# Performance work log

Measured on AMD Instinct MI355X. Metric: run time of the kernel, lower is better.

Reference implementation:

```python
import jax, jax.numpy as jnp
import numpy as np

VOCAB, EMB, HID, NCLS, B, T = 50000, 32, 64, 3, 512, 512

def setup_inputs() -> dict:
    key = jax.random.key(0)
    ks = jax.random.split(key, 7)
    tokens = jax.random.randint(ks[0], (B, T), 0, VOCAB, dtype=jnp.int32)
    emb = jax.random.normal(ks[1], (VOCAB, EMB), dtype=jnp.float32) * 0.05
    # Keras LSTM weights: kernel [EMB, 4*HID], recurrent_kernel [HID, 4*HID], bias [4*HID]; gate order i,f,c,o
    Wk = jax.random.normal(ks[2], (EMB, 4 * HID), dtype=jnp.float32) * (1.0 / np.sqrt(EMB))
    Wr = jax.random.normal(ks[3], (HID, 4 * HID), dtype=jnp.float32) * (1.0 / np.sqrt(HID))
    b = jnp.zeros((4 * HID,), dtype=jnp.float32)
    Wd = jax.random.normal(ks[4], (HID, NCLS), dtype=jnp.float32) * (1.0 / np.sqrt(HID))
    bd = jnp.zeros((NCLS,), dtype=jnp.float32)
    return {"tokens": tokens, "emb": emb, "Wk": Wk, "Wr": Wr, "b": b, "Wd": Wd, "bd": bd}

def _lstm_last_hidden(x, Wk, Wr, b):
    # x: [B, T, EMB] -> last hidden state [B, HID]. Keras gate order: i, f, c(g), o.
    Bsz = x.shape[0]
    # Precompute input projections for all timesteps (one big GEMM): [T, B, 4H]
    xz = jnp.einsum('bte,eh->tbh', x, Wk) + b

    def step(carry, xzt):
        h, c = carry
        z = xzt + h @ Wr  # [B, 4H]
        i, f, g, o = jnp.split(z, 4, axis=-1)
        i = jax.nn.sigmoid(i)
        f = jax.nn.sigmoid(f)
        o = jax.nn.sigmoid(o)
        c = f * c + i * jnp.tanh(g)
        h = o * jnp.tanh(c)
        return (h, c), None

    h0 = jnp.zeros((Bsz, HID), dtype=x.dtype)
    c0 = jnp.zeros((Bsz, HID), dtype=x.dtype)
    (hT, _), _ = jax.lax.scan(step, (h0, c0), xz)
    return hT

def reference(tokens, emb, Wk, Wr, b, Wd, bd):
    x = emb[tokens]                      # [B, T, EMB] embedding lookup
    h = _lstm_last_hidden(x, Wk, Wr, b)  # [B, HID]
    # Dropout layers are identity at inference; Dense + softmax
    logits = h @ Wd + bd                 # [B, NCLS]
    return jax.nn.softmax(logits, axis=-1)
```

## Files before the change

### kernel.cpp

```cpp
#include <hip/hip_runtime.h>


#define VOCAB 50000
#define EMB 32
#define HID 64
#define NCLS 3
#define BATCH 512
#define TSEQ 512
#define FOURH 256
#define LOG2E 1.4426950408889634f
#define GSEQ 4
#define NBLK (BATCH / GSEQ)

typedef _Float16 half8 __attribute__((ext_vector_type(8)));
typedef float f32x4 __attribute__((ext_vector_type(4)));

#define MFMA16 __builtin_amdgcn_mfma_f32_16x16x32_f16
#define PKRTZ(a, b) __builtin_bit_cast(int, __builtin_amdgcn_cvt_pkrtz((a), (b)))

#define LSTM_STEP(CUR, TT, XW, XL)                                            \
    {                                                                         \
        const half8* ap = (const half8*)(hxc + (CUR) * 768 + abase);          \
        const half8 a0 = ap[0];                                               \
        const half8 a1 = ap[4];                                               \
        const half8 a2 = ap[8];                                               \
        if (li8) {                                                            \
            int2 st;                                                          \
            st.x = PKRTZ(XW.x, XW.y);                                         \
            st.y = PKRTZ(XW.z, XW.w);                                         \
            *(int2*)(hxc + ((CUR) ^ 1) * 768 + xwoff) = st;                   \
            const int tn2 = ((TT) + 2 < TSEQ) ? (TT) + 2 : TSEQ - 1;          \
            const int tk = toks[(w << 9) + tn2];                              \
            XL = *(const float4*)(emb + tk * EMB + (l << 2));                 \
        }                                                                     \
        f32x4 ac0, ac1, ac2, ac3;                                             \
        ac0 = MFMA16(a0, bfr[0][0], zz, 0, 0, 0);                             \
        ac1 = MFMA16(a0, bfr[1][0], zz, 0, 0, 0);                             \
        ac2 = MFMA16(a0, bfr[2][0], zz, 0, 0, 0);                             \
        ac3 = MFMA16(a0, bfr[3][0], zz, 0, 0, 0);                             \
        ac0 = MFMA16(a1, bfr[0][1], ac0, 0, 0, 0);                            \
        ac1 = MFMA16(a1, bfr[1][1], ac1, 0, 0, 0);                            \
        ac2 = MFMA16(a1, bfr[2][1], ac2, 0, 0, 0);                            \
        ac3 = MFMA16(a1, bfr[3][1], ac3, 0, 0, 0);                            \
        ac0 = MFMA16(a2, bfr[0][2], ac0, 0, 0, 0);                            \
        ac1 = MFMA16(a2, bfr[1][2], ac1, 0, 0, 0);                            \
        ac2 = MFMA16(a2, bfr[2][2], ac2, 0, 0, 0);                            \
        ac3 = MFMA16(a2, bfr[3][2], ac3, 0, 0, 0);                            \
        const float zi = ac0[0], zf = ac1[0], zg = ac2[0], zo = ac3[0];       \
        const float si = __builtin_amdgcn_rcpf(                               \
            1.0f + __builtin_amdgcn_exp2f(fmaf(zi, -LOG2E, bci)));            \
        const float sf = __builtin_amdgcn_rcpf(                               \
            1.0f + __builtin_amdgcn_exp2f(fmaf(zf, -LOG2E, bcf)));            \
        const float sg = __builtin_amdgcn_rcpf(                               \
            1.0f + __builtin_amdgcn_exp2f(fmaf(zg, -2.0f * LOG2E, bcg)));     \
        const float so = __builtin_amdgcn_rcpf(                               \
            1.0f + __builtin_amdgcn_exp2f(fmaf(zo, -LOG2E, bco)));            \
        const float gt = fmaf(2.0f, sg, -1.0f);                               \
        cst = fmaf(sf, cst, si * gt);                                         \
        const float st2 = __builtin_amdgcn_rcpf(                              \
            1.0f + __builtin_amdgcn_exp2f(cst * (-2.0f * LOG2E)));            \
        const float th = fmaf(2.0f, st2, -1.0f);                              \
        const float hv = so * th;                                             \
        *(_Float16*)(hxc + ((CUR) ^ 1) * 768 + hwoff) = (_Float16)hv;         \
        __syncthreads();                                                      \
    }

__global__ __launch_bounds__(256)
void lstm_kernel(const int* __restrict__ tokens, const float* __restrict__ emb,
                 const float* __restrict__ Wk, const float* __restrict__ Wr,
                 const float* __restrict__ bias, const float* __restrict__ Wd,
                 const float* __restrict__ bd, float* __restrict__ out)
{
    __shared__ __align__(16) _Float16 hx[2][GSEQ][96];
    __shared__ int toks[GSEQ * TSEQ];

    const int tid = threadIdx.x;
    const int w   = tid >> 6;
    const int l   = tid & 63;
    const int li  = l & 15;
    const int q   = l >> 4;
    const bool li8 = (l < 8);
    const int s0  = blockIdx.x << 2;

    char* hxc = (char*)&hx[0][0][0];

    {
        const int4* src = (const int4*)(tokens + (s0 << 9));
        int4* dst = (int4*)toks;
        dst[tid] = src[tid];
        dst[tid + 256] = src[tid + 256];
    }

    if (tid < 64) {
        int2 z2; z2.x = 0; z2.y = 0;
        *(int2*)(hxc + (tid >> 4) * 192 + ((tid & 15) << 3)) = z2;
    }

    half8 bfr[4][3];
#pragma unroll
    for (int g = 0; g < 4; ++g) {
        const int col = (g << 6) + (w << 4) + li;
#pragma unroll
        for (int c2 = 0; c2 < 3; ++c2) {
#pragma unroll
            for (int i = 0; i < 8; ++i) {
                const int k = (c2 << 5) + (q << 3) + i;
                const float wv = (k < HID) ? Wr[k * FOURH + col]
                                           : Wk[(k - HID) * FOURH + col];
                bfr[g][c2][i] = (_Float16)wv;
            }
        }
    }

    const int u = (w << 4) + li;
    const float bci = -bias[u] * LOG2E;
    const float bcf = -bias[u + 64] * LOG2E;
    const float bcg = -bias[u + 128] * (2.0f * LOG2E);
    const float bco = -bias[u + 192] * LOG2E;

    const int abase = ((li >> 2) * 192) + (q << 4);
    const int hwoff = q * 192 + (u << 1);
    const int xwoff = w * 192 + 128 + (l << 3);

    __syncthreads();

    float4 xA = make_float4(0.f, 0.f, 0.f, 0.f);
    float4 xB = make_float4(0.f, 0.f, 0.f, 0.f);
    if (li8) {
        const int tk0 = toks[w << 9];
        const float4 x0 = *(const float4*)(emb + tk0 * EMB + (l << 2));
        int2 st;
        st.x = PKRTZ(x0.x, x0.y);
        st.y = PKRTZ(x0.z, x0.w);
        *(int2*)(hxc + xwoff) = st;
        const int tk1 = toks[(w << 9) + 1];
        xA = *(const float4*)(emb + tk1 * EMB + (l << 2));
    }
    __syncthreads();

    float cst = 0.0f;
    const f32x4 zz = {0.0f, 0.0f, 0.0f, 0.0f};

    for (int t = 0; t < TSEQ; t += 2) {
        LSTM_STEP(0, t, xA, xB)
        LSTM_STEP(1, t + 1, xB, xA)
    }

    if (tid < GSEQ) {
        const _Float16* hf = &hx[0][tid][0];
        float a0 = bd[0], a1 = bd[1], a2 = bd[2];
#pragma unroll 8
        for (int k = 0; k < HID; ++k) {
            const float hk = (float)hf[k];
            a0 = fmaf(hk, Wd[k * NCLS + 0], a0);
            a1 = fmaf(hk, Wd[k * NCLS + 1], a1);
            a2 = fmaf(hk, Wd[k * NCLS + 2], a2);
        }
        const float mm = fmaxf(a0, fmaxf(a1, a2));
        const float e0 = __expf(a0 - mm);
        const float e1 = __expf(a1 - mm);
        const float e2 = __expf(a2 - mm);
        const float den = e0 + e1 + e2;
        float* op = out + (s0 + tid) * NCLS;
        op[0] = e0 / den;
        op[1] = e1 / den;
        op[2] = e2 / den;
    }
}

extern "C" void kernel_launch(void* const* d_in, const int* in_sizes, int n_in,
                              void* d_out, int out_size, void* d_ws, size_t ws_size,
                              hipStream_t stream) {
    const int*   tokens = (const int*)  d_in[0];
    const float* emb    = (const float*)d_in[1];
    const float* Wk     = (const float*)d_in[2];
    const float* Wr     = (const float*)d_in[3];
    const float* b      = (const float*)d_in[4];
    const float* Wd     = (const float*)d_in[5];
    const float* bd     = (const float*)d_in[6];
    float* out = (float*)d_out;
    (void)d_ws; (void)ws_size; (void)in_sizes; (void)n_in; (void)out_size;

    lstm_kernel<<<dim3(NBLK), dim3(256), 0, stream>>>(
        tokens, emb, Wk, Wr, b, Wd, bd, out);
}
```

Before: 229.4 us.

## Split LSTM gate columns across eight waves with swizzle exchange per step

Each block now runs 512 threads (8 waves) instead of 4. Each wave computes two MFMA column tiles, down from four, with every tile holding two gates for 8 hidden units. A ds_swizzle xor-8 exchange lets each lane collect all four gate preactivations. The aim is to halve the serial MFMA chain per timestep on the recurrence critical path. The cost is a cross-lane swizzle per step, a barrier across twice as many waves, and duplicated elementwise work in half the lanes.

```diff
diff --git a/kernel.cpp b/kernel.cpp
--- a/kernel.cpp
+++ b/kernel.cpp
@@ -17,6 +17,12 @@
 
 #define MFMA16 __builtin_amdgcn_mfma_f32_16x16x32_f16
 #define PKRTZ(a, b) __builtin_bit_cast(int, __builtin_amdgcn_cvt_pkrtz((a), (b)))
+#define SWZ_XOR8 0x201F
+
+__device__ __forceinline__ float swz8(float x) {
+    return __builtin_bit_cast(float,
+        __builtin_amdgcn_ds_swizzle(__builtin_bit_cast(int, x), SWZ_XOR8));
+}
 
 #define LSTM_STEP(CUR, TT, XW, XL)                                            \
     {                                                                         \
@@ -24,29 +30,31 @@
         const half8 a0 = ap[0];                                               \
         const half8 a1 = ap[4];                                               \
         const half8 a2 = ap[8];                                               \
-        if (li8) {                                                            \
+        if (stg) {                                                            \
             int2 st;                                                          \
             st.x = PKRTZ(XW.x, XW.y);                                         \
             st.y = PKRTZ(XW.z, XW.w);                                         \
             *(int2*)(hxc + ((CUR) ^ 1) * 768 + xwoff) = st;                   \
+        }                                                                     \
+        f32x4 t0, t1;                                                         \
+        t0 = MFMA16(a0, bfr[0][0], zz, 0, 0, 0);                              \
+        t1 = MFMA16(a0, bfr[1][0], zz, 0, 0, 0);                              \
+        t0 = MFMA16(a1, bfr[0][1], t0, 0, 0, 0);                              \
+        t1 = MFMA16(a1, bfr[1][1], t1, 0, 0, 0);                              \
+        t0 = MFMA16(a2, bfr[0][2], t0, 0, 0, 0);                              \
+        t1 = MFMA16(a2, bfr[1][2], t1, 0, 0, 0);                              \
+        if (stg) {                                                            \
             const int tn2 = ((TT) + 2 < TSEQ) ? (TT) + 2 : TSEQ - 1;          \
             const int tk = toks[(w << 9) + tn2];                              \
             XL = *(const float4*)(emb + tk * EMB + (l << 2));                 \
         }                                                                     \
-        f32x4 ac0, ac1, ac2, ac3;                                             \
-        ac0 = MFMA16(a0, bfr[0][0], zz, 0, 0, 0);                             \
-        ac1 = MFMA16(a0, bfr[1][0], zz, 0, 0, 0);                             \
-        ac2 = MFMA16(a0, bfr[2][0], zz, 0, 0, 0);                             \
-        ac3 = MFMA16(a0, bfr[3][0], zz, 0, 0, 0);                             \
-        ac0 = MFMA16(a1, bfr[0][1], ac0, 0, 0, 0);                            \
-        ac1 = MFMA16(a1, bfr[1][1], ac1, 0, 0, 0);                            \
-        ac2 = MFMA16(a1, bfr[2][1], ac2, 0, 0, 0);                            \
-        ac3 = MFMA16(a1, bfr[3][1], ac3, 0, 0, 0);                            \
-        ac0 = MFMA16(a2, bfr[0][2], ac0, 0, 0, 0);                            \
-        ac1 = MFMA16(a2, bfr[1][2], ac1, 0, 0, 0);                            \
-        ac2 = MFMA16(a2, bfr[2][2], ac2, 0, 0, 0);                            \
-        ac3 = MFMA16(a2, bfr[3][2], ac3, 0, 0, 0);                            \
-        const float zi = ac0[0], zf = ac1[0], zg = ac2[0], zo = ac3[0];       \
+        const float own0 = t0[0], own1 = t1[0];                               \
+        const float oth0 = swz8(own0);                                        \
+        const float oth1 = swz8(own1);                                        \
+        const float zi = b3 ? oth0 : own0;                                    \
+        const float zf = b3 ? own0 : oth0;                                    \
+        const float zg = b3 ? oth1 : own1;                                    \
+        const float zo = b3 ? own1 : oth1;                                    \
         const float si = __builtin_amdgcn_rcpf(                               \
             1.0f + __builtin_amdgcn_exp2f(fmaf(zi, -LOG2E, bci)));            \
         const float sf = __builtin_amdgcn_rcpf(                               \
@@ -59,13 +67,12 @@
         cst = fmaf(sf, cst, si * gt);                                         \
         const float st2 = __builtin_amdgcn_rcpf(                              \
             1.0f + __builtin_amdgcn_exp2f(cst * (-2.0f * LOG2E)));            \
-        const float th = fmaf(2.0f, st2, -1.0f);                              \
-        const float hv = so * th;                                             \
-        *(_Float16*)(hxc + ((CUR) ^ 1) * 768 + hwoff) = (_Float16)hv;         \
+        const float hv = so * fmaf(2.0f, st2, -1.0f);                         \
+        if (!b3) *(_Float16*)(hxc + ((CUR) ^ 1) * 768 + hwoff) = (_Float16)hv;\
         __syncthreads();                                                      \
     }
 
-__global__ __launch_bounds__(256)
+__global__ __launch_bounds__(512)
 void lstm_kernel(const int* __restrict__ tokens, const float* __restrict__ emb,
                  const float* __restrict__ Wk, const float* __restrict__ Wr,
                  const float* __restrict__ bias, const float* __restrict__ Wd,
@@ -79,16 +86,15 @@
     const int l   = tid & 63;
     const int li  = l & 15;
     const int q   = l >> 4;
-    const bool li8 = (l < 8);
+    const int b3  = (l >> 3) & 1;
+    const bool stg = (w < 4) && (l < 8);
     const int s0  = blockIdx.x << 2;
 
     char* hxc = (char*)&hx[0][0][0];
 
     {
-        const int4* src = (const int4*)(tokens + (s0 << 9));
-        int4* dst = (int4*)toks;
-        dst[tid] = src[tid];
-        dst[tid + 256] = src[tid + 256];
+        const int4* src = (const int4*)(tokens + ((long)s0 << 9));
+        ((int4*)toks)[tid] = src[tid];
     }
 
     if (tid < 64) {
@@ -96,10 +102,11 @@
         *(int2*)(hxc + (tid >> 4) * 192 + ((tid & 15) << 3)) = z2;
     }
 
-    half8 bfr[4][3];
+    half8 bfr[2][3];
 #pragma unroll
-    for (int g = 0; g < 4; ++g) {
-        const int col = (g << 6) + (w << 4) + li;
+    for (int tau = 0; tau < 2; ++tau) {
+        const int gate = (tau << 1) + (li >> 3);
+        const int col = (gate << 6) + (w << 3) + (li & 7);
 #pragma unroll
         for (int c2 = 0; c2 < 3; ++c2) {
 #pragma unroll
@@ -107,26 +114,26 @@
                 const int k = (c2 << 5) + (q << 3) + i;
                 const float wv = (k < HID) ? Wr[k * FOURH + col]
                                            : Wk[(k - HID) * FOURH + col];
-                bfr[g][c2][i] = (_Float16)wv;
+                bfr[tau][c2][i] = (_Float16)wv;
             }
         }
     }
 
-    const int u = (w << 4) + li;
+    const int u = (w << 3) + (l & 7);
     const float bci = -bias[u] * LOG2E;
     const float bcf = -bias[u + 64] * LOG2E;
     const float bcg = -bias[u + 128] * (2.0f * LOG2E);
     const float bco = -bias[u + 192] * LOG2E;
 
     const int abase = ((li >> 2) * 192) + (q << 4);
-    const int hwoff = q * 192 + (u << 1);
+    const int hwoff = (l >> 4) * 192 + (u << 1);
     const int xwoff = w * 192 + 128 + (l << 3);
 
     __syncthreads();
 
     float4 xA = make_float4(0.f, 0.f, 0.f, 0.f);
     float4 xB = make_float4(0.f, 0.f, 0.f, 0.f);
-    if (li8) {
+    if (stg) {
         const int tk0 = toks[w << 9];
         const float4 x0 = *(const float4*)(emb + tk0 * EMB + (l << 2));
         int2 st;
@@ -181,6 +188,6 @@
     float* out = (float*)d_out;
     (void)d_ws; (void)ws_size; (void)in_sizes; (void)n_in; (void)out_size;
 
-    lstm_kernel<<<dim3(NBLK), dim3(256), 0, stream>>>(
+    lstm_kernel<<<dim3(NBLK), dim3(512), 0, stream>>>(
         tokens, emb, Wk, Wr, b, Wd, bd, out);
 }
```

Result: slower. 279.4 us (+21.8%).

## Precompute per-vocab input projection table and feed it as MFMA accumulator

Applied to the files above, without the earlier changes.

Adds a pre-pass kernel that computes emb@Wk+b for every vocabulary entry into a workspace table (50000x256 floats), rebuilt on every call. The recurrent kernel then loads the precomputed gate pre-activations per token and uses them as the initial MFMA accumulator. This removes one third of the MFMAs and the per-step embedding staging into LDS from the serial loop. The barrier is changed to an LDS-waitcnt plus s_barrier. The cost is a ~51MB table write and scattered 16-byte reads, and the path only runs when the workspace is large enough.

```diff
diff --git a/kernel.cpp b/kernel.cpp
--- a/kernel.cpp
+++ b/kernel.cpp
@@ -18,35 +18,82 @@
 #define MFMA16 __builtin_amdgcn_mfma_f32_16x16x32_f16
 #define PKRTZ(a, b) __builtin_bit_cast(int, __builtin_amdgcn_cvt_pkrtz((a), (b)))
 
-#define LSTM_STEP(CUR, TT, XW, XL)                                            \
+#define WAVE_BARRIER()                                        \
+    {                                                         \
+        asm volatile("s_waitcnt lgkmcnt(0)" ::: "memory");    \
+        __builtin_amdgcn_s_barrier();                         \
+    }
+
+__global__ __launch_bounds__(256)
+void build_table(const float* __restrict__ emb, const float* __restrict__ Wk,
+                 const float* __restrict__ bias, float* __restrict__ table) {
+    const int c = threadIdx.x;
+    const int u = c >> 2, g = c & 3;
+    const int wi = (g << 6) + u;
+    const float bb = bias[wi];
+    float wcol[EMB];
+#pragma unroll
+    for (int k = 0; k < EMB; ++k) wcol[k] = Wk[k * FOURH + wi];
+    for (int v = blockIdx.x; v < VOCAB; v += gridDim.x) {
+        const float4* er = (const float4*)(emb + (long)v * EMB);
+        float acc = bb;
+#pragma unroll
+        for (int kk = 0; kk < EMB / 4; ++kk) {
+            const float4 e = er[kk];
+            acc = fmaf(e.x, wcol[kk * 4 + 0], acc);
+            acc = fmaf(e.y, wcol[kk * 4 + 1], acc);
+            acc = fmaf(e.z, wcol[kk * 4 + 2], acc);
+            acc = fmaf(e.w, wcol[kk * 4 + 3], acc);
+        }
+        table[(long)v * FOURH + c] = acc;
+    }
+}
+
+#define LSTM_STEP(CUR, TT, ZX, TK, XW, XL)                                    \
     {                                                                         \
         const half8* ap = (const half8*)(hxc + (CUR) * 768 + abase);          \
         const half8 a0 = ap[0];                                               \
         const half8 a1 = ap[4];                                               \
-        const half8 a2 = ap[8];                                               \
-        if (li8) {                                                            \
-            int2 st;                                                          \
-            st.x = PKRTZ(XW.x, XW.y);                                         \
-            st.y = PKRTZ(XW.z, XW.w);                                         \
-            *(int2*)(hxc + ((CUR) ^ 1) * 768 + xwoff) = st;                   \
-            const int tn2 = ((TT) + 2 < TSEQ) ? (TT) + 2 : TSEQ - 1;          \
-            const int tk = toks[(w << 9) + tn2];                              \
-            XL = *(const float4*)(emb + tk * EMB + (l << 2));                 \
+        f32x4 ac0, ac1, ac2, ac3;                                             \
+        if constexpr (TAB) {                                                  \
+            ac0 = MFMA16(a0, bfr[0][0], ZX, 0, 0, 0);                         \
+            ac1 = MFMA16(a0, bfr[1][0], ZX, 0, 0, 0);                         \
+            ac2 = MFMA16(a0, bfr[2][0], ZX, 0, 0, 0);                         \
+            ac3 = MFMA16(a0, bfr[3][0], ZX, 0, 0, 0);                         \
+        } else {                                                              \
+            ac0 = MFMA16(a0, bfr[0][0], zz, 0, 0, 0);                         \
+            ac1 = MFMA16(a0, bfr[1][0], zz, 0, 0, 0);                         \
+            ac2 = MFMA16(a0, bfr[2][0], zz, 0, 0, 0);                         \
+            ac3 = MFMA16(a0, bfr[3][0], zz, 0, 0, 0);                         \
         }                                                                     \
-        f32x4 ac0, ac1, ac2, ac3;                                             \
-        ac0 = MFMA16(a0, bfr[0][0], zz, 0, 0, 0);                             \
-        ac1 = MFMA16(a0, bfr[1][0], zz, 0, 0, 0);                             \
-        ac2 = MFMA16(a0, bfr[2][0], zz, 0, 0, 0);                             \
-        ac3 = MFMA16(a0, bfr[3][0], zz, 0, 0, 0);                             \
         ac0 = MFMA16(a1, bfr[0][1], ac0, 0, 0, 0);                            \
         ac1 = MFMA16(a1, bfr[1][1], ac1, 0, 0, 0);                            \
         ac2 = MFMA16(a1, bfr[2][1], ac2, 0, 0, 0);                            \
         ac3 = MFMA16(a1, bfr[3][1], ac3, 0, 0, 0);                            \
-        ac0 = MFMA16(a2, bfr[0][2], ac0, 0, 0, 0);                            \
-        ac1 = MFMA16(a2, bfr[1][2], ac1, 0, 0, 0);                            \
-        ac2 = MFMA16(a2, bfr[2][2], ac2, 0, 0, 0);                            \
-        ac3 = MFMA16(a2, bfr[3][2], ac3, 0, 0, 0);                            \
-        const float zi = ac0[0], zf = ac1[0], zg = ac2[0], zo = ac3[0];       \
+        if constexpr (TAB) {                                                  \
+            ZX = *(const f32x4*)(table + (long)(TK) * FOURH + (u << 2));      \
+            const int tn4 = ((TT) + 4 < TSEQ) ? (TT) + 4 : TSEQ - 1;          \
+            TK = toks[(q << 9) + tn4];                                        \
+        } else {                                                              \
+            const half8 a2 = ap[8];                                           \
+            ac0 = MFMA16(a2, bfr[0][2], ac0, 0, 0, 0);                        \
+            ac1 = MFMA16(a2, bfr[1][2], ac1, 0, 0, 0);                        \
+            ac2 = MFMA16(a2, bfr[2][2], ac2, 0, 0, 0);                        \
+            ac3 = MFMA16(a2, bfr[3][2], ac3, 0, 0, 0);                        \
+            if (li8) {                                                        \
+                int2 st;                                                      \
+                st.x = PKRTZ(XW.x, XW.y);                                     \
+                st.y = PKRTZ(XW.z, XW.w);                                     \
+                *(int2*)(hxc + ((CUR) ^ 1) * 768 + xwoff) = st;               \
+                const int tn2 = ((TT) + 2 < TSEQ) ? (TT) + 2 : TSEQ - 1;      \
+                const int tk2 = toks[(w << 9) + tn2];                         \
+                XL = *(const float4*)(emb + (long)tk2 * EMB + (l << 2));      \
+            }                                                                 \
+        }                                                                     \
+        const float zi = ac0[0];                                              \
+        const float zf = ac1[1];                                              \
+        const float zg = ac2[2];                                              \
+        const float zo = ac3[3];                                              \
         const float si = __builtin_amdgcn_rcpf(                               \
             1.0f + __builtin_amdgcn_exp2f(fmaf(zi, -LOG2E, bci)));            \
         const float sf = __builtin_amdgcn_rcpf(                               \
@@ -59,17 +106,18 @@
         cst = fmaf(sf, cst, si * gt);                                         \
         const float st2 = __builtin_amdgcn_rcpf(                              \
             1.0f + __builtin_amdgcn_exp2f(cst * (-2.0f * LOG2E)));            \
-        const float th = fmaf(2.0f, st2, -1.0f);                              \
-        const float hv = so * th;                                             \
+        const float hv = so * fmaf(2.0f, st2, -1.0f);                         \
         *(_Float16*)(hxc + ((CUR) ^ 1) * 768 + hwoff) = (_Float16)hv;         \
-        __syncthreads();                                                      \
-    }
-
+        WAVE_BARRIER()                                                        \
+    }
+
+template <bool TAB>
 __global__ __launch_bounds__(256)
 void lstm_kernel(const int* __restrict__ tokens, const float* __restrict__ emb,
                  const float* __restrict__ Wk, const float* __restrict__ Wr,
                  const float* __restrict__ bias, const float* __restrict__ Wd,
-                 const float* __restrict__ bd, float* __restrict__ out)
+                 const float* __restrict__ bd, const float* __restrict__ table,
+                 float* __restrict__ out)
 {
     __shared__ __align__(16) _Float16 hx[2][GSEQ][96];
     __shared__ int toks[GSEQ * TSEQ];
@@ -85,9 +133,9 @@
     char* hxc = (char*)&hx[0][0][0];
 
     {
-        const int4* src = (const int4*)(tokens + (s0 << 9));
+        const int4* src = (const int4*)(tokens + ((long)s0 << 9));
         int4* dst = (int4*)toks;
-        dst[tid] = src[tid];
+        dst[tid]       = src[tid];
         dst[tid + 256] = src[tid + 256];
     }
 
@@ -101,22 +149,19 @@
     for (int g = 0; g < 4; ++g) {
         const int col = (g << 6) + (w << 4) + li;
 #pragma unroll
-        for (int c2 = 0; c2 < 3; ++c2) {
-#pragma unroll
-            for (int i = 0; i < 8; ++i) {
-                const int k = (c2 << 5) + (q << 3) + i;
-                const float wv = (k < HID) ? Wr[k * FOURH + col]
-                                           : Wk[(k - HID) * FOURH + col];
-                bfr[g][c2][i] = (_Float16)wv;
-            }
+        for (int i = 0; i < 8; ++i) {
+            const int kq = (q << 3) + i;
+            bfr[g][0][i] = (_Float16)Wr[kq * FOURH + col];
+            bfr[g][1][i] = (_Float16)Wr[(32 + kq) * FOURH + col];
+            if constexpr (!TAB) bfr[g][2][i] = (_Float16)Wk[kq * FOURH + col];
         }
     }
 
     const int u = (w << 4) + li;
-    const float bci = -bias[u] * LOG2E;
-    const float bcf = -bias[u + 64] * LOG2E;
-    const float bcg = -bias[u + 128] * (2.0f * LOG2E);
-    const float bco = -bias[u + 192] * LOG2E;
+    const float bci = TAB ? 0.0f : -bias[u] * LOG2E;
+    const float bcf = TAB ? 0.0f : -bias[u + 64] * LOG2E;
+    const float bcg = TAB ? 0.0f : -bias[u + 128] * (2.0f * LOG2E);
+    const float bco = TAB ? 0.0f : -bias[u + 192] * LOG2E;
 
     const int abase = ((li >> 2) * 192) + (q << 4);
     const int hwoff = q * 192 + (u << 1);
@@ -124,17 +169,28 @@
 
     __syncthreads();
 
+    f32x4 zxA{}, zxB{};
+    int tkA = 0, tkB = 0;
     float4 xA = make_float4(0.f, 0.f, 0.f, 0.f);
     float4 xB = make_float4(0.f, 0.f, 0.f, 0.f);
-    if (li8) {
-        const int tk0 = toks[w << 9];
-        const float4 x0 = *(const float4*)(emb + tk0 * EMB + (l << 2));
-        int2 st;
-        st.x = PKRTZ(x0.x, x0.y);
-        st.y = PKRTZ(x0.z, x0.w);
-        *(int2*)(hxc + xwoff) = st;
-        const int tk1 = toks[(w << 9) + 1];
-        xA = *(const float4*)(emb + tk1 * EMB + (l << 2));
+    if constexpr (TAB) {
+        const int t0 = toks[(q << 9) + 0];
+        const int t1 = toks[(q << 9) + 1];
+        zxA = *(const f32x4*)(table + (long)t0 * FOURH + (u << 2));
+        zxB = *(const f32x4*)(table + (long)t1 * FOURH + (u << 2));
+        tkA = toks[(q << 9) + 2];
+        tkB = toks[(q << 9) + 3];
+    } else {
+        if (li8) {
+            const int tk0 = toks[w << 9];
+            const float4 x0 = *(const float4*)(emb + (long)tk0 * EMB + (l << 2));
+            int2 st;
+            st.x = PKRTZ(x0.x, x0.y);
+            st.y = PKRTZ(x0.z, x0.w);
+            *(int2*)(hxc + xwoff) = st;
+            const int tk1 = toks[(w << 9) + 1];
+            xA = *(const float4*)(emb + (long)tk1 * EMB + (l << 2));
+        }
     }
     __syncthreads();
 
@@ -142,8 +198,8 @@
     const f32x4 zz = {0.0f, 0.0f, 0.0f, 0.0f};
 
     for (int t = 0; t < TSEQ; t += 2) {
-        LSTM_STEP(0, t, xA, xB)
-        LSTM_STEP(1, t + 1, xB, xA)
+        LSTM_STEP(0, t,     zxA, tkA, xA, xB)
+        LSTM_STEP(1, t + 1, zxB, tkB, xB, xA)
     }
 
     if (tid < GSEQ) {
@@ -179,8 +235,16 @@
     const float* Wd     = (const float*)d_in[5];
     const float* bd     = (const float*)d_in[6];
     float* out = (float*)d_out;
-    (void)d_ws; (void)ws_size; (void)in_sizes; (void)n_in; (void)out_size;
-
-    lstm_kernel<<<dim3(NBLK), dim3(256), 0, stream>>>(
-        tokens, emb, Wk, Wr, b, Wd, bd, out);
+    (void)in_sizes; (void)n_in; (void)out_size;
+
+    const size_t need = (size_t)VOCAB * FOURH * sizeof(float);
+    if (ws_size >= need) {
+        float* table = (float*)d_ws;
+        build_table<<<dim3(2048), dim3(256), 0, stream>>>(emb, Wk, b, table);
+        lstm_kernel<true><<<dim3(NBLK), dim3(256), 0, stream>>>(
+            tokens, emb, Wk, Wr, b, Wd, bd, table, out);
+    } else {
+        lstm_kernel<false><<<dim3(NBLK), dim3(256), 0, stream>>>(
+            tokens, emb, Wk, Wr, b, Wd, bd, nullptr, out);
+    }
 }
```

Result: faster. 201.3 us (-12.2%).
